# Kernel tuning notes

Measured on AMD Instinct MI355X. Metric: run time of the kernel, lower is better.

## Reference

```python
import jax, jax.numpy as jnp
import numpy as np

B, T, C = 8, 8192, 512

def setup_inputs() -> dict:
    key = jax.random.key(0)
    x = jax.random.normal(key, (B, T, C), dtype=jnp.float32)
    return {"x": x}

def reference(x) -> jnp.ndarray:
    # Causal bag-of-words: out[b, t] = mean(x[b, :t+1]).
    # Equivalent to softmax over zero logits with a causal mask, then matmul,
    # but computed as an O(T*C) cumulative mean instead of an O(T^2*C) matmul.
    csum = jnp.cumsum(x, axis=1)                                  # (B, T, C)
    counts = jnp.arange(1, x.shape[1] + 1, dtype=x.dtype)[None, :, None]
    return csum / counts
```

## Files before the change

kernel.cpp:

```cpp
#include <hip/hip_runtime.h>


constexpr int B   = 8;
constexpr int T   = 8192;
constexpr int C   = 512;
constexpr int C4  = C / 4;
constexpr int L   = 32;
constexpr int NCH = T / L;

typedef float f32x4 __attribute__((ext_vector_type(4)));

__device__ __forceinline__ float4 f4add(float4 a, float4 b) {
    return make_float4(a.x + b.x, a.y + b.y, a.z + b.z, a.w + b.w);
}

__global__ __launch_bounds__(256) void cbow_chunksums(
        const float4* __restrict__ x, float4* __restrict__ ws) {
    const int tid   = blockIdx.x * blockDim.x + threadIdx.x;
    const int c4    = tid & (C4 - 1);
    const int chunk = (tid >> 7) & (NCH - 1);
    const int b     = tid >> 15;

    const float4* p = x + ((b * T) + chunk * L) * C4 + c4;
    float4 s = make_float4(0.f, 0.f, 0.f, 0.f);
    float4 buf[8];
    for (int tt = 0; tt < L; tt += 8) {
#pragma unroll
        for (int k = 0; k < 8; ++k) buf[k] = p[(tt + k) * C4];
#pragma unroll
        for (int k = 0; k < 8; ++k) s = f4add(s, buf[k]);
    }
    ws[(b * NCH + chunk) * C4 + c4] = s;
}

__global__ __launch_bounds__(256) void cbow_wscan(float4* __restrict__ ws) {
    const int bc = blockIdx.x;
    const int b  = bc >> 7;
    const int c4 = bc & (C4 - 1);
    const int t  = threadIdx.x;

    __shared__ float4 sm[NCH];

    float4 v = ws[(b * NCH + t) * C4 + c4];
    sm[t] = v;
    __syncthreads();

#pragma unroll
    for (int off = 1; off < NCH; off <<= 1) {
        float4 tmp = (t >= off) ? sm[t - off]
                                : make_float4(0.f, 0.f, 0.f, 0.f);
        __syncthreads();
        v = f4add(v, tmp);
        sm[t] = v;
        __syncthreads();
    }

    const float4 excl = (t > 0) ? sm[t - 1] : make_float4(0.f, 0.f, 0.f, 0.f);
    ws[(b * NCH + t) * C4 + c4] = excl;
}

__global__ __launch_bounds__(256) void cbow_scan(
        const float4* __restrict__ x, const float4* __restrict__ ws,
        float4* __restrict__ out) {
    const int tid   = blockIdx.x * blockDim.x + threadIdx.x;
    const int c4    = tid & (C4 - 1);
    const int chunk = (tid >> 7) & (NCH - 1);
    const int b     = tid >> 15;

    float4 run = ws[(b * NCH + chunk) * C4 + c4];

    const int     base = ((b * T) + chunk * L) * C4 + c4;
    const float4* p    = x + base;
    float4*       o    = out + base;
    const int     t0   = chunk * L;

    float4 buf[8];
    for (int tt = 0; tt < L; tt += 8) {
#pragma unroll
        for (int k = 0; k < 8; ++k) buf[k] = p[(tt + k) * C4];
#pragma unroll
        for (int k = 0; k < 8; ++k) {
            run = f4add(run, buf[k]);
            const float inv = __builtin_amdgcn_rcpf((float)(t0 + tt + k + 1));
            f32x4 val = {run.x * inv, run.y * inv, run.z * inv, run.w * inv};
            __builtin_nontemporal_store(val, (f32x4*)(o + (tt + k) * C4));
        }
    }
}

extern "C" void kernel_launch(void* const* d_in, const int* in_sizes, int n_in,
                              void* d_out, int out_size, void* d_ws, size_t ws_size,
                              hipStream_t stream) {
    const float4* x   = (const float4*)d_in[0];
    float4*       out = (float4*)d_out;
    float4*       ws  = (float4*)d_ws;

    const int n_threads = B * NCH * C4;
    const int block = 256;
    const int grid  = n_threads / block;

    cbow_chunksums<<<grid, block, 0, stream>>>(x, ws);
    cbow_wscan<<<B * C4, block, 0, stream>>>(ws);
    cbow_scan<<<grid, block, 0, stream>>>(x, ws, out);
}
```

Baseline: 258.3 us.

## Fuse chunk-sum scan into final pass via per-block carry reduction

Removes the separate chunk-sum scan kernel; each scan block instead sums all preceding chunk totals from the workspace to get its carry. Both remaining kernels are remapped so one block handles one (batch, chunk) with two row groups exchanging partials through shared memory. This saves a launch and a global round-trip, but adds quadratic redundant workspace reads that are expected to be served from cache, and creates load imbalance for late chunks.

```diff
diff --git a/kernel.cpp b/kernel.cpp
--- a/kernel.cpp
+++ b/kernel.cpp
@@ -1,12 +1,13 @@
 #include <hip/hip_runtime.h>
 
 
-constexpr int B   = 8;
-constexpr int T   = 8192;
-constexpr int C   = 512;
-constexpr int C4  = C / 4;
-constexpr int L   = 32;
-constexpr int NCH = T / L;
+constexpr int B    = 8;
+constexpr int T    = 8192;
+constexpr int C    = 512;
+constexpr int C4   = C / 4;
+constexpr int L    = 32;
+constexpr int NCH  = T / L;
+constexpr int NBLK = B * NCH;
 
 typedef float f32x4 __attribute__((ext_vector_type(4)));
 
@@ -14,77 +15,91 @@
     return make_float4(a.x + b.x, a.y + b.y, a.z + b.z, a.w + b.w);
 }
 
-__global__ __launch_bounds__(256) void cbow_chunksums(
+__global__ __launch_bounds__(256) void cbow_sums(
         const float4* __restrict__ x, float4* __restrict__ ws) {
-    const int tid   = blockIdx.x * blockDim.x + threadIdx.x;
-    const int c4    = tid & (C4 - 1);
-    const int chunk = (tid >> 7) & (NCH - 1);
-    const int b     = tid >> 15;
+    const int g     = blockIdx.x;
+    const int b     = g >> 8;
+    const int chunk = g & (NCH - 1);
+    const int t     = threadIdx.x;
 
-    const float4* p = x + ((b * T) + chunk * L) * C4 + c4;
-    float4 s = make_float4(0.f, 0.f, 0.f, 0.f);
+    const size_t base = ((size_t)(b * T) + (size_t)chunk * L) * C4;
+    const float4* p = x + base + t;
+
+    float4 acc = make_float4(0.f, 0.f, 0.f, 0.f);
     float4 buf[8];
-    for (int tt = 0; tt < L; tt += 8) {
 #pragma unroll
-        for (int k = 0; k < 8; ++k) buf[k] = p[(tt + k) * C4];
+    for (int h = 0; h < 2; ++h) {
 #pragma unroll
-        for (int k = 0; k < 8; ++k) s = f4add(s, buf[k]);
-    }
-    ws[(b * NCH + chunk) * C4 + c4] = s;
-}
-
-__global__ __launch_bounds__(256) void cbow_wscan(float4* __restrict__ ws) {
-    const int bc = blockIdx.x;
-    const int b  = bc >> 7;
-    const int c4 = bc & (C4 - 1);
-    const int t  = threadIdx.x;
-
-    __shared__ float4 sm[NCH];
-
-    float4 v = ws[(b * NCH + t) * C4 + c4];
-    sm[t] = v;
-    __syncthreads();
-
+        for (int k = 0; k < 8; ++k) buf[k] = p[(h * 8 + k) * 256];
 #pragma unroll
-    for (int off = 1; off < NCH; off <<= 1) {
-        float4 tmp = (t >= off) ? sm[t - off]
-                                : make_float4(0.f, 0.f, 0.f, 0.f);
-        __syncthreads();
-        v = f4add(v, tmp);
-        sm[t] = v;
-        __syncthreads();
+        for (int k = 0; k < 8; ++k) acc = f4add(acc, buf[k]);
     }
 
-    const float4 excl = (t > 0) ? sm[t - 1] : make_float4(0.f, 0.f, 0.f, 0.f);
-    ws[(b * NCH + t) * C4 + c4] = excl;
+    __shared__ float4 part[2][C4];
+    part[t >> 7][t & (C4 - 1)] = acc;
+    __syncthreads();
+    if (t < C4) {
+        ws[(size_t)(b * NCH + chunk) * C4 + t] = f4add(part[0][t], part[1][t]);
+    }
 }
 
 __global__ __launch_bounds__(256) void cbow_scan(
         const float4* __restrict__ x, const float4* __restrict__ ws,
         float4* __restrict__ out) {
-    const int tid   = blockIdx.x * blockDim.x + threadIdx.x;
-    const int c4    = tid & (C4 - 1);
-    const int chunk = (tid >> 7) & (NCH - 1);
-    const int b     = tid >> 15;
+    const int g     = blockIdx.x;
+    const int b     = g >> 8;
+    const int chunk = g & (NCH - 1);
+    const int t     = threadIdx.x;
+    const int c4    = t & (C4 - 1);
+    const int rg    = t >> 7;
 
-    float4 run = ws[(b * NCH + chunk) * C4 + c4];
+    __shared__ float4 lp[2][C4];
+    __shared__ float4 ls[2][2][C4];
 
-    const int     base = ((b * T) + chunk * L) * C4 + c4;
-    const float4* p    = x + base;
-    float4*       o    = out + base;
-    const int     t0   = chunk * L;
+    const float4* w = ws + (size_t)b * NCH * C4 + c4;
+    float4 a0 = make_float4(0.f, 0.f, 0.f, 0.f);
+    float4 a1 = a0, a2 = a0, a3 = a0;
+    int j = rg;
+    for (; j + 6 < chunk; j += 8) {
+        a0 = f4add(a0, w[(size_t)(j + 0) * C4]);
+        a1 = f4add(a1, w[(size_t)(j + 2) * C4]);
+        a2 = f4add(a2, w[(size_t)(j + 4) * C4]);
+        a3 = f4add(a3, w[(size_t)(j + 6) * C4]);
+    }
+    for (; j < chunk; j += 2) a0 = f4add(a0, w[(size_t)j * C4]);
+    lp[rg][c4] = f4add(f4add(a0, a1), f4add(a2, a3));
+    __syncthreads();
+    float4 carry = f4add(lp[0][c4], lp[1][c4]);
+
+    const size_t base = ((size_t)(b * T) + (size_t)chunk * L) * C4;
+    const float4* p = x + base;
+    float4*       o = out + base;
 
     float4 buf[8];
-    for (int tt = 0; tt < L; tt += 8) {
 #pragma unroll
-        for (int k = 0; k < 8; ++k) buf[k] = p[(tt + k) * C4];
+    for (int m = 0; m < 2; ++m) {
+        const int r0 = m * 16 + rg * 8;
+#pragma unroll
+        for (int k = 0; k < 8; ++k) buf[k] = p[(size_t)(r0 + k) * C4 + c4];
+
+        float4 s8 = buf[0];
+#pragma unroll
+        for (int k = 1; k < 8; ++k) s8 = f4add(s8, buf[k]);
+        ls[m][rg][c4] = s8;
+        __syncthreads();
+
+        float4 run = carry;
+        if (rg) run = f4add(run, ls[m][0][c4]);
+
+        const int trow = chunk * L + r0;
 #pragma unroll
         for (int k = 0; k < 8; ++k) {
             run = f4add(run, buf[k]);
-            const float inv = __builtin_amdgcn_rcpf((float)(t0 + tt + k + 1));
+            const float inv = __builtin_amdgcn_rcpf((float)(trow + k + 1));
             f32x4 val = {run.x * inv, run.y * inv, run.z * inv, run.w * inv};
-            __builtin_nontemporal_store(val, (f32x4*)(o + (tt + k) * C4));
+            __builtin_nontemporal_store(val, (f32x4*)(o + (size_t)(r0 + k) * C4 + c4));
         }
+        carry = f4add(carry, f4add(ls[m][0][c4], ls[m][1][c4]));
     }
 }
 
@@ -95,11 +110,6 @@
     float4*       out = (float4*)d_out;
     float4*       ws  = (float4*)d_ws;
 
-    const int n_threads = B * NCH * C4;
-    const int block = 256;
-    const int grid  = n_threads / block;
-
-    cbow_chunksums<<<grid, block, 0, stream>>>(x, ws);
-    cbow_wscan<<<B * C4, block, 0, stream>>>(ws);
-    cbow_scan<<<grid, block, 0, stream>>>(x, ws, out);
+    cbow_sums<<<NBLK, 256, 0, stream>>>(x, ws);
+    cbow_scan<<<NBLK, 256, 0, stream>>>(x, ws, out);
 }
```

After: 266.3 us. 1.03x slower.
